# Performance work log

Measured on AMD Instinct MI355X. Metric: run time of the kernel, lower is better.

The kernel has to match this reference:

```python
import jax, jax.numpy as jnp
import numpy as np

B, T, D = 16, 512, 8576
STD = 0.05
MEAN = 0.0
EPS = 1e-5  # torch BatchNorm1d default


def setup_inputs() -> dict:
    key = jax.random.key(0)
    k1, k2 = jax.random.split(key)
    x = jax.random.normal(k1, (B, T, D), dtype=jnp.float32)
    noise = jax.random.normal(k2, (B, T, D), dtype=jnp.float32)
    gamma = jnp.ones((D,), dtype=jnp.float32)
    beta = jnp.zeros((D,), dtype=jnp.float32)
    return {"x": x, "noise": noise, "gamma": gamma, "beta": beta}


def reference(x, noise, gamma, beta):
    # BatchNorm1d in training mode: stats over (batch, time) per channel D.
    # Original does x.transpose(1,2) -> BN over dim -> transpose back; with
    # channel-last layout that is just per-channel normalization over axes (0,1).
    mu = jnp.mean(x, axis=(0, 1))                      # [D]
    var = jnp.mean(jnp.square(x - mu), axis=(0, 1))    # biased variance, [D]
    xn = (x - mu) * jax.lax.rsqrt(var + EPS)
    y = xn * gamma + beta
    # additive Gaussian noise: randn * std + mean
    return y + (noise * STD + MEAN)
```

## Files before the change

### kernel.cpp

```cpp
#include <hip/hip_runtime.h>

#define N_ROWS 8192
#define D_CH   8576
#define DV     (D_CH / 4)
#define MAX_CHUNKS 256
#define APPLY_ROWS_PER_BLOCK 16
#define APPLY_ROW_CHUNKS (N_ROWS / APPLY_ROWS_PER_BLOCK)
#define EPSV 1e-5f
#define NOISE_STD 0.05f

typedef float f32x4 __attribute__((ext_vector_type(4)));


__global__ __launch_bounds__(256) void bn_partial_stats(
    const f32x4* __restrict__ x, f32x4* __restrict__ part, int rows_per_block)
{
    int vc = blockIdx.x * blockDim.x + threadIdx.x;
    if (vc >= DV) return;
    size_t base = (size_t)blockIdx.y * rows_per_block * DV + vc;
    f32x4 s0 = (f32x4)0.f, s1 = (f32x4)0.f, s2 = (f32x4)0.f, s3 = (f32x4)0.f;
    f32x4 q0 = (f32x4)0.f, q1 = (f32x4)0.f, q2 = (f32x4)0.f, q3 = (f32x4)0.f;
    for (int r = 0; r < rows_per_block; r += 8) {
        size_t b = base + (size_t)r * DV;
        f32x4 v0 = x[b + 0 * (size_t)DV];
        f32x4 v1 = x[b + 1 * (size_t)DV];
        f32x4 v2 = x[b + 2 * (size_t)DV];
        f32x4 v3 = x[b + 3 * (size_t)DV];
        f32x4 v4 = x[b + 4 * (size_t)DV];
        f32x4 v5 = x[b + 5 * (size_t)DV];
        f32x4 v6 = x[b + 6 * (size_t)DV];
        f32x4 v7 = x[b + 7 * (size_t)DV];
        s0 += v0; q0 += v0 * v0;
        s1 += v1; q1 += v1 * v1;
        s2 += v2; q2 += v2 * v2;
        s3 += v3; q3 += v3 * v3;
        s0 += v4; q0 += v4 * v4;
        s1 += v5; q1 += v5 * v5;
        s2 += v6; q2 += v6 * v6;
        s3 += v7; q3 += v7 * v7;
    }
    f32x4 s = (s0 + s1) + (s2 + s3);
    f32x4 q = (q0 + q1) + (q2 + q3);
    size_t slot = (size_t)blockIdx.y * (2 * DV) + vc;
    part[slot]      = s;
    part[slot + DV] = q;
}

__global__ __launch_bounds__(256) void bn_finalize(
    const f32x4* __restrict__ part,
    const f32x4* __restrict__ gamma4, const f32x4* __restrict__ beta4,
    f32x4* __restrict__ ws_scale, f32x4* __restrict__ ws_shift, int nchunks)
{
    int vc = blockIdx.x * blockDim.x + threadIdx.x;
    if (vc >= DV) return;
    f32x4 s = (f32x4)0.f, q = (f32x4)0.f;
    for (int c = 0; c < nchunks; c += 4) {
        size_t b0 = (size_t)(c + 0) * (2 * DV) + vc;
        size_t b1 = (size_t)(c + 1) * (2 * DV) + vc;
        size_t b2 = (size_t)(c + 2) * (2 * DV) + vc;
        size_t b3 = (size_t)(c + 3) * (2 * DV) + vc;
        f32x4 sa = part[b0], qa = part[b0 + DV];
        f32x4 sb = part[b1], qb = part[b1 + DV];
        f32x4 sc_ = part[b2], qc = part[b2 + DV];
        f32x4 sd = part[b3], qd = part[b3 + DV];
        s += (sa + sb) + (sc_ + sd);
        q += (qa + qb) + (qc + qd);
    }
    const float invN = 1.0f / (float)N_ROWS;
    f32x4 mu = s * invN;
    f32x4 var = q * invN - mu * mu;
    f32x4 gm = gamma4[vc];
    f32x4 bt = beta4[vc];
    f32x4 sc;
    sc.x = gm.x * rsqrtf(var.x + EPSV);
    sc.y = gm.y * rsqrtf(var.y + EPSV);
    sc.z = gm.z * rsqrtf(var.z + EPSV);
    sc.w = gm.w * rsqrtf(var.w + EPSV);
    ws_scale[vc] = sc;
    ws_shift[vc] = bt - mu * sc;
}

__global__ __launch_bounds__(256) void bn_apply(
    const f32x4* __restrict__ x, const f32x4* __restrict__ noise,
    const f32x4* __restrict__ ws_scale4, const f32x4* __restrict__ ws_shift4,
    f32x4* __restrict__ out)
{
    int vc = blockIdx.x * blockDim.x + threadIdx.x;
    if (vc >= DV) return;
    f32x4 sc = ws_scale4[vc];
    f32x4 sh = ws_shift4[vc];
    size_t base = (size_t)blockIdx.y * APPLY_ROWS_PER_BLOCK * DV + vc;
#pragma unroll
    for (int h = 0; h < 2; ++h) {
        size_t b = base + (size_t)(h * 8) * DV;
        f32x4 xv[8], nv[8];
#pragma unroll
        for (int r = 0; r < 8; ++r) {
            xv[r] = x[b + (size_t)r * DV];
            nv[r] = __builtin_nontemporal_load(&noise[b + (size_t)r * DV]);
        }
#pragma unroll
        for (int r = 0; r < 8; ++r) {
            f32x4 o = xv[r] * sc + sh + nv[r] * NOISE_STD;
            __builtin_nontemporal_store(o, &out[b + (size_t)r * DV]);
        }
    }
}

extern "C" void kernel_launch(void* const* d_in, const int* in_sizes, int n_in,
                              void* d_out, int out_size, void* d_ws, size_t ws_size,
                              hipStream_t stream) {
    const float* x     = (const float*)d_in[0];
    const float* noise = (const float*)d_in[1];
    const float* gamma = (const float*)d_in[2];
    const float* beta  = (const float*)d_in[3];
    float* out = (float*)d_out;

    int nchunks = MAX_CHUNKS;
    while (nchunks > 4 &&
           ((size_t)nchunks * 2 * DV + 2 * DV) * sizeof(f32x4) > ws_size)
        nchunks >>= 1;
    int rows_per_block = N_ROWS / nchunks;

    f32x4* part     = (f32x4*)d_ws;
    f32x4* ws_scale = part + (size_t)nchunks * 2 * DV;
    f32x4* ws_shift = ws_scale + DV;

    dim3 blk(256, 1, 1);
    dim3 grd_stats((DV + 255) / 256, nchunks, 1);
    bn_partial_stats<<<grd_stats, blk, 0, stream>>>((const f32x4*)x, part, rows_per_block);

    dim3 grd_fin((DV + 255) / 256, 1, 1);
    bn_finalize<<<grd_fin, blk, 0, stream>>>(part, (const f32x4*)gamma, (const f32x4*)beta,
                                             ws_scale, ws_shift, nchunks);

    dim3 grd_apply((DV + 255) / 256, APPLY_ROW_CHUNKS, 1);
    bn_apply<<<grd_apply, blk, 0, stream>>>((const f32x4*)x, (const f32x4*)noise,
                                            (const f32x4*)ws_scale, (const f32x4*)ws_shift,
                                            (f32x4*)out);
}
```

Before: 223.5 us.

## Split statistics finalization into a parallel two-level reduction

Adds an intermediate reduction kernel that collapses per-chunk partial sums into 16 groups across many blocks, so the finalize kernel only sums 16 partials instead of looping over all chunks with just a handful of blocks. The chunk count for the first stats pass is also halved, shrinking the partial-sum buffer. This targets the low-parallelism serial tail of the reduction at the cost of one extra kernel launch and a second small workspace buffer.

```diff
diff --git a/kernel.cpp b/kernel.cpp
--- a/kernel.cpp
+++ b/kernel.cpp
@@ -3,7 +3,8 @@
 #define N_ROWS 8192
 #define D_CH   8576
 #define DV     (D_CH / 4)
-#define MAX_CHUNKS 256
+#define NCHUNKS_MAX 128
+#define NRED 16
 #define APPLY_ROWS_PER_BLOCK 16
 #define APPLY_ROW_CHUNKS (N_ROWS / APPLY_ROWS_PER_BLOCK)
 #define EPSV 1e-5f
@@ -46,23 +47,44 @@
     part[slot + DV] = q;
 }
 
-__global__ __launch_bounds__(256) void bn_finalize(
-    const f32x4* __restrict__ part,
-    const f32x4* __restrict__ gamma4, const f32x4* __restrict__ beta4,
-    f32x4* __restrict__ ws_scale, f32x4* __restrict__ ws_shift, int nchunks)
+__global__ __launch_bounds__(256) void bn_reduce(
+    const f32x4* __restrict__ part, f32x4* __restrict__ part2, int factor)
 {
     int vc = blockIdx.x * blockDim.x + threadIdx.x;
     if (vc >= DV) return;
     f32x4 s = (f32x4)0.f, q = (f32x4)0.f;
-    for (int c = 0; c < nchunks; c += 4) {
+    int c0 = blockIdx.y * factor;
+    for (int g = 0; g < factor; g += 2) {
+        size_t b0 = (size_t)(c0 + g) * (2 * DV) + vc;
+        size_t b1 = (size_t)(c0 + g + 1) * (2 * DV) + vc;
+        f32x4 sa = part[b0], qa = part[b0 + DV];
+        f32x4 sb = part[b1], qb = part[b1 + DV];
+        s += sa + sb;
+        q += qa + qb;
+    }
+    size_t o = (size_t)blockIdx.y * (2 * DV) + vc;
+    part2[o]      = s;
+    part2[o + DV] = q;
+}
+
+__global__ __launch_bounds__(256) void bn_finalize(
+    const f32x4* __restrict__ part2,
+    const f32x4* __restrict__ gamma4, const f32x4* __restrict__ beta4,
+    f32x4* __restrict__ ws_scale, f32x4* __restrict__ ws_shift)
+{
+    int vc = blockIdx.x * blockDim.x + threadIdx.x;
+    if (vc >= DV) return;
+    f32x4 s = (f32x4)0.f, q = (f32x4)0.f;
+#pragma unroll
+    for (int c = 0; c < NRED; c += 4) {
         size_t b0 = (size_t)(c + 0) * (2 * DV) + vc;
         size_t b1 = (size_t)(c + 1) * (2 * DV) + vc;
         size_t b2 = (size_t)(c + 2) * (2 * DV) + vc;
         size_t b3 = (size_t)(c + 3) * (2 * DV) + vc;
-        f32x4 sa = part[b0], qa = part[b0 + DV];
-        f32x4 sb = part[b1], qb = part[b1 + DV];
-        f32x4 sc_ = part[b2], qc = part[b2 + DV];
-        f32x4 sd = part[b3], qd = part[b3 + DV];
+        f32x4 sa = part2[b0], qa = part2[b0 + DV];
+        f32x4 sb = part2[b1], qb = part2[b1 + DV];
+        f32x4 sc_ = part2[b2], qc = part2[b2 + DV];
+        f32x4 sd = part2[b3], qd = part2[b3 + DV];
         s += (sa + sb) + (sc_ + sd);
         q += (qa + qb) + (qc + qd);
     }
@@ -116,23 +138,27 @@
     const float* beta  = (const float*)d_in[3];
     float* out = (float*)d_out;
 
-    int nchunks = MAX_CHUNKS;
-    while (nchunks > 4 &&
-           ((size_t)nchunks * 2 * DV + 2 * DV) * sizeof(f32x4) > ws_size)
+    int nchunks = NCHUNKS_MAX;
+    while (nchunks > NRED &&
+           ((size_t)(nchunks + NRED) * 2 * DV + 2 * DV) * sizeof(f32x4) > ws_size)
         nchunks >>= 1;
     int rows_per_block = N_ROWS / nchunks;
 
     f32x4* part     = (f32x4*)d_ws;
-    f32x4* ws_scale = part + (size_t)nchunks * 2 * DV;
+    f32x4* part2    = part + (size_t)nchunks * 2 * DV;
+    f32x4* ws_scale = part2 + (size_t)NRED * 2 * DV;
     f32x4* ws_shift = ws_scale + DV;
 
     dim3 blk(256, 1, 1);
     dim3 grd_stats((DV + 255) / 256, nchunks, 1);
     bn_partial_stats<<<grd_stats, blk, 0, stream>>>((const f32x4*)x, part, rows_per_block);
 
+    dim3 grd_red((DV + 255) / 256, NRED, 1);
+    bn_reduce<<<grd_red, blk, 0, stream>>>(part, part2, nchunks / NRED);
+
     dim3 grd_fin((DV + 255) / 256, 1, 1);
-    bn_finalize<<<grd_fin, blk, 0, stream>>>(part, (const f32x4*)gamma, (const f32x4*)beta,
-                                             ws_scale, ws_shift, nchunks);
+    bn_finalize<<<grd_fin, blk, 0, stream>>>(part2, (const f32x4*)gamma, (const f32x4*)beta,
+                                             ws_scale, ws_shift);
 
     dim3 grd_apply((DV + 255) / 256, APPLY_ROW_CHUNKS, 1);
     bn_apply<<<grd_apply, blk, 0, stream>>>((const f32x4*)x, (const f32x4*)noise,
```

Result: faster. 180.4 us, median of 2 (-19.3%).
